# Kernel tuning notes

Hardware: AMD Instinct MI355X
Metric: run time of the kernel (lower is better)

## Reference

```python
import jax, jax.numpy as jnp
import numpy as np

B, S, D = 4, 2048, 768
H = 12
HD = D // H  # 64
SCALE = HD ** -0.5

def setup_inputs() -> dict:
    key = jax.random.key(0)
    k1, k2, k3 = jax.random.split(key, 3)
    x = jax.random.normal(k1, (B, S, D), dtype=jnp.float32)
    w_qkv = jax.random.normal(k2, (D, 3 * D), dtype=jnp.float32) * (D ** -0.5)
    w_out = jax.random.normal(k3, (D, D), dtype=jnp.float32) * (D ** -0.5)
    b_out = jnp.zeros((D,), dtype=jnp.float32)
    return {"x": x, "w_qkv": w_qkv, "w_out": w_out, "b_out": b_out}

def reference(x, w_qkv, w_out, b_out):
    B_, S_, D_ = x.shape
    # qkv projection (no bias), then 'b s (qkv h d) -> qkv b h s d'
    qkv = (x @ w_qkv).reshape(B_, S_, 3, H, HD).transpose(2, 0, 3, 1, 4)
    q, k, v = qkv[0], qkv[1], qkv[2]  # each [B, H, S, HD]
    att = jnp.einsum('bhxd,bhyd->bhxy', q, k) * SCALE
    att = jax.nn.softmax(att, axis=-1)  # dropout_rate=0 -> identity
    out = jnp.einsum('bhxy,bhyd->bhxd', att, v)
    out = out.transpose(0, 2, 1, 3).reshape(B_, S_, D_)  # 'b h s d -> b s (h d)'
    return out @ w_out + b_out
```

## Files before the change

### kernel.cpp

```cpp
#include <hip/hip_runtime.h>

#define BB 4
#define SS 2048
#define DD 768
#define HH 12
#define HDIM 64

using bf16_t = __bf16;
typedef __bf16 bf16x8 __attribute__((ext_vector_type(8)));
typedef __bf16 bf16x4 __attribute__((ext_vector_type(4)));
typedef __bf16 bf16x2 __attribute__((ext_vector_type(2)));
typedef float f32x4 __attribute__((ext_vector_type(4)));
typedef float f32x16 __attribute__((ext_vector_type(16)));
typedef unsigned int u32;
typedef unsigned int u32x4 __attribute__((ext_vector_type(4)));

static __device__ __forceinline__ void cp16(void* lds, const void* g) {
  __builtin_amdgcn_global_load_lds(
      (const __attribute__((address_space(1))) u32*)g,
      (__attribute__((address_space(3))) u32*)lds, 16, 0, 0);
}

__global__ void cvt_x(const float* __restrict__ in, bf16_t* __restrict__ out) {
  const size_t i = ((size_t)blockIdx.x * 256 + threadIdx.x) * 8;
  f32x4 f0 = *(const f32x4*)(in + i);
  f32x4 f1 = *(const f32x4*)(in + i + 4);
  bf16x8 v;
#pragma unroll
  for (int j = 0; j < 4; j++) { v[j] = (bf16_t)f0[j]; v[4 + j] = (bf16_t)f1[j]; }
  *(bf16x8*)(out + i) = v;
}

__global__ void wt_transpose(const float* __restrict__ in, bf16_t* __restrict__ out,
                             int K, int N) {
  __shared__ bf16_t tile[64][65];
  const int n0 = blockIdx.x * 64, k0 = blockIdx.y * 64;
  const int t = threadIdx.x;
  const int r = t >> 2;
  const int c0 = (t & 3) * 16;
  const float* src = in + (size_t)(k0 + r) * N + n0 + c0;
#pragma unroll
  for (int q = 0; q < 4; q++) {
    f32x4 f = *(const f32x4*)(src + q * 4);
#pragma unroll
    for (int j = 0; j < 4; j++) tile[r][c0 + q * 4 + j] = (bf16_t)f[j];
  }
  __syncthreads();
  bf16x8 o0, o1;
#pragma unroll
  for (int j = 0; j < 8; j++) { o0[j] = tile[c0 + j][r]; o1[j] = tile[c0 + 8 + j][r]; }
  *(bf16x8*)(out + (size_t)(n0 + r) * K + k0 + c0) = o0;
  *(bf16x8*)(out + (size_t)(n0 + r) * K + k0 + c0 + 8) = o1;
}

template <int MODE>
__global__ __launch_bounds__(256, 2)
void gemm_bt(const bf16_t* __restrict__ A, const bf16_t* __restrict__ Bt,
             int M, int N, int K,
             bf16_t* __restrict__ q_out, bf16_t* __restrict__ k_out,
             bf16_t* __restrict__ vt_out,
             float* __restrict__ Cout, const float* __restrict__ bias) {
  __shared__ bf16_t As[2][128][64];
  __shared__ bf16_t Bs[2][128][64];
  const int t = threadIdx.x;
  const int lane = t & 63, wave = t >> 6;
  const int l15 = lane & 15, quad = lane >> 4;
  const int wm = (wave >> 1) * 64, wn = (wave & 1) * 64;

  const int nx = gridDim.x;
  const int L = blockIdx.y * nx + blockIdx.x;
  const int chunk = (nx * gridDim.y) >> 3;
  const int v = (L & 7) * chunk + (L >> 3);
  const int m0 = (v / nx) * 128, n0 = (v % nx) * 128;

  const int srow = lane >> 3;
  const int schunk = ((lane & 7) ^ srow) * 8;
  const int rsw = l15 & 7;

  f32x4 acc[4][4];
#pragma unroll
  for (int i = 0; i < 4; i++)
#pragma unroll
    for (int j = 0; j < 4; j++) acc[i][j] = (f32x4){0.f, 0.f, 0.f, 0.f};

  auto stage = [&](int k0, int buf) {
#pragma unroll
    for (int p = 0; p < 4; p++) {
      const int row = wave * 32 + p * 8 + srow;
      const bf16_t* asrc;
      if (MODE == 0) {
        asrc = A + (size_t)(m0 + row) * K + k0 + schunk;
      } else {
        const int mm = m0 + row, b = mm >> 11, s = mm & 2047, h = k0 >> 6;
        asrc = A + (((size_t)(b * HH + h)) * SS + s) * HDIM + schunk;
      }
      cp16(&As[buf][wave * 32 + p * 8][0], asrc);
      cp16(&Bs[buf][wave * 32 + p * 8][0],
           Bt + (size_t)(n0 + row) * K + k0 + schunk);
    }
  };

  const int NT = K / 64;
  stage(0, 0);

  for (int kt = 0; kt < NT; kt++) {
    const int buf = kt & 1;
    __syncthreads();
    if (kt + 1 < NT) stage((kt + 1) * 64, buf ^ 1);
#pragma unroll
    for (int kk = 0; kk < 2; kk++) {
      bf16x8 af[4], bfr[4];
#pragma unroll
      for (int i = 0; i < 4; i++)
        af[i] = *(const bf16x8*)&As[buf][wm + i * 16 + l15][((kk * 4 + quad) ^ rsw) * 8];
#pragma unroll
      for (int j = 0; j < 4; j++)
        bfr[j] = *(const bf16x8*)&Bs[buf][wn + j * 16 + l15][((kk * 4 + quad) ^ rsw) * 8];
#pragma unroll
      for (int i = 0; i < 4; i++)
#pragma unroll
        for (int j = 0; j < 4; j++)
          acc[i][j] = __builtin_amdgcn_mfma_f32_16x16x32_bf16(af[i], bfr[j], acc[i][j], 0, 0, 0);
    }
  }

  const float QSCALE = 0.125f * 1.44269504088896340736f;
#pragma unroll
  for (int i = 0; i < 4; i++) {
    const int mbase = m0 + wm + i * 16 + quad * 4;
#pragma unroll
    for (int j = 0; j < 4; j++) {
      const int n = n0 + wn + j * 16 + l15;
#pragma unroll
      for (int r = 0; r < 4; r++) {
        const float v = acc[i][j][r];
        const int mm = mbase + r;
        if (MODE == 0) {
          const int sel = n / DD;
          const int rem = n - sel * DD;
          const int h = rem >> 6, d = rem & 63;
          const int b = mm >> 11, s = mm & 2047;
          if (sel == 2) {
            vt_out[((size_t)(b * HH + h) * HDIM + d) * SS + s] = (bf16_t)v;
          } else {
            const size_t idx = (((size_t)(b * HH + h)) * SS + s) * HDIM + d;
            if (sel == 0) q_out[idx] = (bf16_t)(v * QSCALE);
            else k_out[idx] = (bf16_t)v;
          }
        } else {
          Cout[(size_t)mm * N + n] = v + bias[n];
        }
      }
    }
  }
}

__global__ __launch_bounds__(256, 3)
void attn_kernel(bf16_t* __restrict__ Qio, const bf16_t* __restrict__ Kg,
                 const bf16_t* __restrict__ Vt) {
  __shared__ bf16_t Ks[2][64][64];
  __shared__ bf16_t Vts[2][64][64];
  __shared__ float lsum[128];
  const int t = threadIdx.x;
  const int lane = t & 63, wave = t >> 6;
  const int l31 = lane & 31, hi = lane >> 5;

  const int L = blockIdx.y * gridDim.x + blockIdx.x;
  const int v = (L & 7) * ((16 * BB * HH) / 8) + (L >> 3);
  const int bh = v >> 4;
  const int q0 = (v & 15) * 128;

  const size_t base = (size_t)bh * SS * HDIM;
  const size_t baset = (size_t)bh * HDIM * SS;
  const int wq = wave * 32;
  const int srow = lane >> 3;
  const int schunk = ((lane & 7) ^ srow) * 8;
  const int rsw = l31 & 7;

  bf16x8 qf[4];
#pragma unroll
  for (int kd = 0; kd < 4; kd++)
    qf[kd] = *(const bf16x8*)(Qio + base + (size_t)(q0 + wq + l31) * HDIM +
                              kd * 16 + hi * 8);

  float l_lane = 0.f;
  f32x16 o_acc[2];
#pragma unroll
  for (int dt = 0; dt < 2; dt++)
#pragma unroll
    for (int r = 0; r < 16; r++) o_acc[dt][r] = 0.f;

  auto stage = [&](int k0, int buf) {
#pragma unroll
    for (int p = 0; p < 2; p++) {
      const int row = wave * 16 + p * 8 + srow;
      cp16(&Ks[buf][wave * 16 + p * 8][0],
           Kg + base + (size_t)(k0 + row) * HDIM + schunk);
      cp16(&Vts[buf][wave * 16 + p * 8][0],
           Vt + baset + (size_t)row * SS + k0 + schunk);
    }
  };

  stage(0, 0);

  for (int it = 0; it < SS / 64; it++) {
    const int buf = it & 1;
    __syncthreads();
    if (it + 1 < SS / 64) stage((it + 1) * 64, buf ^ 1);

    f32x16 sT[2];
#pragma unroll
    for (int ct = 0; ct < 2; ct++)
#pragma unroll
      for (int r = 0; r < 16; r++) sT[ct][r] = 0.f;
    __builtin_amdgcn_s_setprio(1);
#pragma unroll
    for (int ct = 0; ct < 2; ct++)
#pragma unroll
      for (int kd = 0; kd < 4; kd++) {
        bf16x8 kf = *(const bf16x8*)&Ks[buf][ct * 32 + l31][((2 * kd + hi) ^ rsw) * 8];
        sT[ct] = __builtin_amdgcn_mfma_f32_32x32x16_bf16(kf, qf[kd], sT[ct], 0, 0, 0);
      }
    __builtin_amdgcn_s_setprio(0);

    bf16x8 pa[4];
#pragma unroll
    for (int ct = 0; ct < 2; ct++) {
      float p[16];
#pragma unroll
      for (int r = 0; r < 16; r++) p[r] = __builtin_amdgcn_exp2f(sT[ct][r]);
#pragma unroll
      for (int r = 0; r < 16; r += 4)
        l_lane += (p[r] + p[r + 1]) + (p[r + 2] + p[r + 3]);
      u32 w[4][2];
#pragma unroll
      for (int g = 0; g < 4; g++)
#pragma unroll
        for (int i = 0; i < 2; i++) {
          bf16x2 pk = {(bf16_t)p[4 * g + 2 * i], (bf16_t)p[4 * g + 2 * i + 1]};
          w[g][i] = *(u32*)&pk;
        }
#pragma unroll
      for (int sub = 0; sub < 2; sub++) {
        u32 a0 = w[2 * sub][0], b0 = w[2 * sub + 1][0];
        u32 a1 = w[2 * sub][1], b1 = w[2 * sub + 1][1];
        asm volatile("v_permlane32_swap_b32 %0, %1" : "+v"(a0), "+v"(b0));
        asm volatile("v_permlane32_swap_b32 %0, %1" : "+v"(a1), "+v"(b1));
        u32x4 fr = {a0, a1, b0, b1};
        pa[ct * 2 + sub] = *(bf16x8*)&fr;
      }
    }

    __builtin_amdgcn_s_setprio(1);
#pragma unroll
    for (int kk = 0; kk < 4; kk++)
#pragma unroll
      for (int dt = 0; dt < 2; dt++) {
        bf16x8 vf = *(const bf16x8*)&Vts[buf][dt * 32 + l31][((2 * kk + hi) ^ rsw) * 8];
        o_acc[dt] = __builtin_amdgcn_mfma_f32_32x32x16_bf16(pa[kk], vf, o_acc[dt], 0, 0, 0);
      }
    __builtin_amdgcn_s_setprio(0);
  }

  const float lf = l_lane + __shfl_xor(l_lane, 32);
  lsum[wq + l31] = lf;
#pragma unroll
  for (int r = 0; r < 16; r++) {
    const int q = wq + (r & 3) + 8 * (r >> 2) + 4 * hi;
    const float inv = 1.0f / lsum[q];
#pragma unroll
    for (int dt = 0; dt < 2; dt++) {
      const int d = dt * 32 + l31;
      Qio[base + (size_t)(q0 + q) * HDIM + d] = (bf16_t)(o_acc[dt][r] * inv);
    }
  }
}

extern "C" void kernel_launch(void* const* d_in, const int* in_sizes, int n_in,
                              void* d_out, int out_size, void* d_ws, size_t ws_size,
                              hipStream_t stream) {
  const float* x = (const float*)d_in[0];
  const float* w_qkv = (const float*)d_in[1];
  const float* w_out = (const float*)d_in[2];
  const float* b_out = (const float*)d_in[3];
  float* out = (float*)d_out;

  char* ws = (char*)d_ws;
  bf16_t* wqkv_t = (bf16_t*)ws; ws += (size_t)3 * DD * DD * 2;
  bf16_t* wout_t = (bf16_t*)ws; ws += (size_t)DD * DD * 2;
  bf16_t* q_ws = (bf16_t*)ws;   ws += (size_t)BB * HH * SS * HDIM * 2;
  bf16_t* k_ws = (bf16_t*)ws;
  bf16_t* vt_sc = (bf16_t*)d_out;
  bf16_t* xb = (bf16_t*)d_out + (size_t)BB * SS * DD;

  cvt_x<<<(BB * SS * DD) / (256 * 8), 256, 0, stream>>>(x, xb);
  wt_transpose<<<dim3(3 * DD / 64, DD / 64), 256, 0, stream>>>(w_qkv, wqkv_t, DD, 3 * DD);
  wt_transpose<<<dim3(DD / 64, DD / 64), 256, 0, stream>>>(w_out, wout_t, DD, DD);
  gemm_bt<0><<<dim3(3 * DD / 128, BB * SS / 128), 256, 0, stream>>>(
      xb, wqkv_t, BB * SS, 3 * DD, DD, q_ws, k_ws, vt_sc, nullptr, nullptr);
  attn_kernel<<<dim3(SS / 128, BB * HH), 256, 0, stream>>>(q_ws, k_ws, vt_sc);
  gemm_bt<1><<<dim3(DD / 128, BB * SS / 128), 256, 0, stream>>>(
      q_ws, wout_t, BB * SS, DD, DD, nullptr, nullptr, nullptr, out, b_out);
}
```

Measured before the change: 228.2 us.

## Software-pipeline attention loop so QK of next tile overlaps softmax and PV

Restructures the flash-attention inner loop into a two-stage software pipeline. K and V get separate staging, the QK^T scores for tile i+1 are computed alongside the exp/PV work for tile i, and the loop is manually unrolled by two with ping-pong score registers. The aim is to overlap MFMA work with the exp/pack/permlane work and to hide LDS load latency. The cost is higher register pressure from two live score accumulators and hardcoded iteration counts tied to S=2048.

```diff
diff --git a/kernel.cpp b/kernel.cpp
--- a/kernel.cpp
+++ b/kernel.cpp
@@ -190,39 +190,37 @@
 #pragma unroll
     for (int r = 0; r < 16; r++) o_acc[dt][r] = 0.f;
 
-  auto stage = [&](int k0, int buf) {
-#pragma unroll
-    for (int p = 0; p < 2; p++) {
-      const int row = wave * 16 + p * 8 + srow;
+  f32x16 sA[2], sB[2];
+
+  auto stageK = [&](int k0, int buf) {
+#pragma unroll
+    for (int p = 0; p < 2; p++)
       cp16(&Ks[buf][wave * 16 + p * 8][0],
-           Kg + base + (size_t)(k0 + row) * HDIM + schunk);
+           Kg + base + (size_t)(k0 + wave * 16 + p * 8 + srow) * HDIM + schunk);
+  };
+  auto stageV = [&](int k0, int buf) {
+#pragma unroll
+    for (int p = 0; p < 2; p++)
       cp16(&Vts[buf][wave * 16 + p * 8][0],
-           Vt + baset + (size_t)row * SS + k0 + schunk);
-    }
-  };
-
-  stage(0, 0);
-
-  for (int it = 0; it < SS / 64; it++) {
-    const int buf = it & 1;
-    __syncthreads();
-    if (it + 1 < SS / 64) stage((it + 1) * 64, buf ^ 1);
-
-    f32x16 sT[2];
-#pragma unroll
-    for (int ct = 0; ct < 2; ct++)
-#pragma unroll
-      for (int r = 0; r < 16; r++) sT[ct][r] = 0.f;
+           Vt + baset + (size_t)(wave * 16 + p * 8 + srow) * SS + k0 + schunk);
+  };
+
+  auto qk = [&](int buf, f32x16 (&s)[2]) {
     __builtin_amdgcn_s_setprio(1);
 #pragma unroll
-    for (int ct = 0; ct < 2; ct++)
+    for (int ct = 0; ct < 2; ct++) {
+#pragma unroll
+      for (int r = 0; r < 16; r++) s[ct][r] = 0.f;
 #pragma unroll
       for (int kd = 0; kd < 4; kd++) {
         bf16x8 kf = *(const bf16x8*)&Ks[buf][ct * 32 + l31][((2 * kd + hi) ^ rsw) * 8];
-        sT[ct] = __builtin_amdgcn_mfma_f32_32x32x16_bf16(kf, qf[kd], sT[ct], 0, 0, 0);
-      }
+        s[ct] = __builtin_amdgcn_mfma_f32_32x32x16_bf16(kf, qf[kd], s[ct], 0, 0, 0);
+      }
+    }
     __builtin_amdgcn_s_setprio(0);
-
+  };
+
+  auto smpv = [&](int buf, const f32x16 (&sT)[2]) {
     bf16x8 pa[4];
 #pragma unroll
     for (int ct = 0; ct < 2; ct++) {
@@ -250,7 +248,6 @@
         pa[ct * 2 + sub] = *(bf16x8*)&fr;
       }
     }
-
     __builtin_amdgcn_s_setprio(1);
 #pragma unroll
     for (int kk = 0; kk < 4; kk++)
@@ -260,7 +257,31 @@
         o_acc[dt] = __builtin_amdgcn_mfma_f32_32x32x16_bf16(pa[kk], vf, o_acc[dt], 0, 0, 0);
       }
     __builtin_amdgcn_s_setprio(0);
-  }
+  };
+
+  stageK(0, 0); stageK(64, 1); stageV(0, 0);
+  __syncthreads();
+  qk(0, sA);
+  __syncthreads();
+
+#pragma unroll 1
+  for (int it = 0; it < 30; it += 2) {
+    stageK((it + 2) * 64, 0);
+    stageV((it + 1) * 64, 1);
+    qk(1, sB);
+    smpv(0, sA);
+    __syncthreads();
+    stageK((it + 3) * 64, 1);
+    stageV((it + 2) * 64, 0);
+    qk(0, sA);
+    smpv(1, sB);
+    __syncthreads();
+  }
+  stageV(31 * 64, 1);
+  qk(1, sB);
+  smpv(0, sA);
+  __syncthreads();
+  smpv(1, sB);
 
   const float lf = l_lane + __shfl_xor(l_lane, 32);
   lsum[wq + l31] = lf;
```

After: 229.1 us. Within noise of the previous version (+0.4%).
